# Optimization experiments

Hardware: AMD Instinct MI355X
Metric: run time of the kernel (lower is better)

The kernel has to match this reference:

```python
import jax, jax.numpy as jnp
import numpy as np
from jax import lax

B, CIN, COUT, H, W = 4, 256, 256, 64, 64
K = 3  # kernel size
PAD = 1
STRIDE = 1


def setup_inputs() -> dict:
    key = jax.random.key(0)
    k1, k2, k3, k4 = jax.random.split(key, 4)
    x = jax.random.normal(k1, (B, CIN, H, W), dtype=jnp.float32)
    # small offset weights so learned offsets are modest (original init is zeros)
    offset_w = jax.random.normal(k2, (3 * K * K, CIN, K, K), dtype=jnp.float32) * 0.01
    offset_b = jax.random.normal(k3, (3 * K * K,), dtype=jnp.float32) * 0.01
    dcn_w = jax.random.normal(k4, (COUT, CIN, K, K), dtype=jnp.float32) * (1.0 / np.sqrt(CIN * K * K))
    return {"x": x, "offset_w": offset_w, "offset_b": offset_b, "dcn_w": dcn_w}


def _dcnv2(x, offset_w, offset_b, dcn_w):
    b, c, h, w = x.shape
    kk = K * K
    # offset conv (standard 3x3, stride 1, pad 1)
    o = lax.conv_general_dilated(
        x, offset_w, (STRIDE, STRIDE), ((PAD, PAD), (PAD, PAD)),
        dimension_numbers=("NCHW", "OIHW", "NCHW"))
    o = o + offset_b[None, :, None, None]
    ho, wo = o.shape[2], o.shape[3]
    off = o[:, : 2 * kk].reshape(b, kk, 2, ho, wo)  # pairs are (dy, dx)
    dy, dx = off[:, :, 0], off[:, :, 1]             # [b,kk,ho,wo]
    mask = jax.nn.sigmoid(o[:, 2 * kk:])            # [b,kk,ho,wo]

    ki, kj = jnp.meshgrid(jnp.arange(K), jnp.arange(K), indexing="ij")
    ki = ki.reshape(kk).astype(jnp.float32)
    kj = kj.reshape(kk).astype(jnp.float32)
    base_y = (jnp.arange(ho, dtype=jnp.float32) * STRIDE - PAD)[None, None, :, None] + ki[None, :, None, None]
    base_x = (jnp.arange(wo, dtype=jnp.float32) * STRIDE - PAD)[None, None, None, :] + kj[None, :, None, None]
    py = base_y + dy  # [b,kk,ho,wo] sampling y
    px = base_x + dx  # sampling x

    y0 = jnp.floor(py)
    x0 = jnp.floor(px)
    wy = py - y0  # bilinear fractional weights
    wx = px - x0
    y0i = y0.astype(jnp.int32)
    x0i = x0.astype(jnp.int32)

    xT = x.transpose(0, 2, 3, 1)  # [b,h,w,c] for channel-last gathers
    bidx = jnp.arange(b)[:, None, None, None]

    def gather(yi, xi):
        # zero padding outside the image
        valid = (yi >= 0) & (yi < h) & (xi >= 0) & (xi < w)
        yc = jnp.clip(yi, 0, h - 1)
        xc = jnp.clip(xi, 0, w - 1)
        v = xT[bidx, yc, xc]  # [b,kk,ho,wo,c]
        return v * valid[..., None].astype(x.dtype)

    g00 = gather(y0i, x0i)
    g01 = gather(y0i, x0i + 1)
    g10 = gather(y0i + 1, x0i)
    g11 = gather(y0i + 1, x0i + 1)

    wy_ = wy[..., None]
    wx_ = wx[..., None]
    sampled = (g00 * (1 - wy_) * (1 - wx_) + g01 * (1 - wy_) * wx_
               + g10 * wy_ * (1 - wx_) + g11 * wy_ * wx_)
    sampled = sampled * mask[..., None]  # modulation

    wk = dcn_w.reshape(dcn_w.shape[0], c, kk)  # [o,c,kk]
    return jnp.einsum("bkhwc,ock->bohw", sampled, wk)


def reference(x, offset_w, offset_b, dcn_w):
    return _dcnv2(x, offset_w, offset_b, dcn_w)
```

## Files before the change

kernel.cpp:

```cpp
#include <hip/hip_runtime.h>
#include <hip/hip_bf16.h>
#include <stdint.h>
#include <math.h>

#define KDIM 2304

typedef __attribute__((ext_vector_type(8))) short bf16x8;
typedef __attribute__((ext_vector_type(4))) float f32x4;

__device__ inline unsigned short f2bf(float f) {
  union { float f; unsigned int u; } v; v.f = f;
  unsigned int u = v.u;
  unsigned int r = (u + 0x7FFFu + ((u >> 16) & 1u)) >> 16;
  return (unsigned short)r;
}
__device__ inline float bf2f(unsigned short h) {
  union { unsigned int u; float f; } v; v.u = ((unsigned int)h) << 16;
  return v.f;
}

__device__ inline void gl2lds16(const void* g, void* l) {
  __builtin_amdgcn_global_load_lds((const __attribute__((address_space(1))) void*)g,
                                   (__attribute__((address_space(3))) void*)l,
                                   16, 0, 0);
}

__global__ __launch_bounds__(256) void k_prep(const float* __restrict__ x,
                                              unsigned short* __restrict__ xTb,
                                              const float* __restrict__ dcn_w,
                                              const float* __restrict__ offset_w,
                                              unsigned short* __restrict__ Wpk,
                                              unsigned short* __restrict__ Wob,
                                              unsigned short* __restrict__ zp) {
  __shared__ float tile[32][33];
  int bx = (int)blockIdx.x;
  int t = threadIdx.x;
  if (bx < 4096) {
    int tx = t & 31, ty = t >> 5;
    int p0 = (bx & 127) * 32;
    int c0 = ((bx >> 7) & 7) * 32;
    int b  = bx >> 10;
    const float* xb = x + ((size_t)b << 20);
#pragma unroll
    for (int i = 0; i < 4; ++i) {
      int c = c0 + ty + i * 8;
      tile[ty + i * 8][tx] = xb[((size_t)c << 12) + p0 + tx];
    }
    __syncthreads();
    unsigned short* ob = xTb + ((size_t)b << 20);
#pragma unroll
    for (int i = 0; i < 4; ++i) {
      int p = p0 + ty + i * 8;
      ob[(((size_t)p) << 8) + c0 + tx] = f2bf(tile[tx][ty + i * 8]);
    }
  } else {
    int gid = (bx - 4096) * 256 + t;
    const int N1 = 72 * 8192;
    const int N2 = 32 * KDIM;
    if (gid < N1) {
      int j = gid & 7;
      int lane = (gid >> 3) & 63;
      int mb = (gid >> 9) & 15;
      int kc = gid >> 13;
      int row = mb * 16 + (lane & 15);
      int gk = kc * 32 + ((lane >> 4) << 3) + j;
      int c = gk & 255, kidx = gk >> 8;
      Wpk[gid] = f2bf(dcn_w[((size_t)(row * 256 + c)) * 9 + kidx]);
    } else if (gid < N1 + N2) {
      int g = gid - N1;
      int ch = g / KDIM, k = g % KDIM;
      int kidx = k >> 8, c = k & 255;
      Wob[g] = (ch < 27) ? f2bf(offset_w[((size_t)(ch * 256 + c)) * 9 + kidx])
                         : (unsigned short)0;
    } else if (gid < N1 + N2 + 128) {
      zp[gid - N1 - N2] = 0;
    }
  }
}

__global__ __launch_bounds__(512) void k_offs(const unsigned short* __restrict__ xTb,
                                              const unsigned short* __restrict__ Wob,
                                              const unsigned short* __restrict__ zp,
                                              const float* __restrict__ offb,
                                              float* __restrict__ SW) {
  __shared__ unsigned short As[2][64 * 32];
  __shared__ unsigned short Bs[2][32 * 32];
  __shared__ float Os[64][33];
  int t = threadIdx.x;
  int wv = t >> 6, lane = t & 63;
  int bid = (int)blockIdx.x;
  int swz = (bid & 7) * 32 + (bid >> 3);
  int n0 = swz * 64;
  int r0 = t >> 2, coff = (t & 3) * 8;

  int rowA = n0 + (r0 & 63);
  int b_ = rowA >> 12, hw = rowA & 4095, h = hw >> 6, w = hw & 63;

  f32x4 acc = {};

  auto stage = [&](int kt, int buf) {
    int k0 = kt * 32;
    int kidx = k0 >> 8, c0 = k0 & 255;
    if (t < 256) {
      int di = kidx / 3 - 1, dj = kidx % 3 - 1;
      int y = h + di, xx = w + dj;
      const unsigned short* g = (y >= 0 && y < 64 && xx >= 0 && xx < 64)
          ? xTb + (((((size_t)b_) << 12) + (y << 6) + xx) << 8) + c0 + coff
          : zp;
      gl2lds16(g, (char*)As[buf] + wv * 1024);
    } else if (t < 384) {
      int tt = t - 256;
      const unsigned short* gB = Wob + (size_t)(tt >> 2) * KDIM + k0 + (tt & 3) * 8;
      gl2lds16(gB, (char*)Bs[buf] + (wv - 4) * 1024);
    }
  };

  stage(0, 0);

  int mf = wv & 3, nf = wv >> 2;
  for (int kt = 0; kt < 72; ++kt) {
    int buf = kt & 1;
    if (kt + 1 < 72) {
      stage(kt + 1, buf ^ 1);
      if (t < 384) asm volatile("s_waitcnt vmcnt(1)" ::: "memory");
      else         asm volatile("s_waitcnt vmcnt(0)" ::: "memory");
    } else {
      asm volatile("s_waitcnt vmcnt(0)" ::: "memory");
    }
    asm volatile("s_barrier" ::: "memory");

    bf16x8 aF = *(const bf16x8*)(As[buf] + (mf * 16 + (lane & 15)) * 32 + (lane >> 4) * 8);
    bf16x8 bF = *(const bf16x8*)(Bs[buf] + (nf * 16 + (lane & 15)) * 32 + (lane >> 4) * 8);
    acc = __builtin_amdgcn_mfma_f32_16x16x32_bf16(aF, bF, acc, 0, 0, 0);

    asm volatile("s_barrier" ::: "memory");
  }

  int quad = lane >> 4, cl = lane & 15;
#pragma unroll
  for (int r = 0; r < 4; ++r)
    Os[mf * 16 + quad * 4 + r][nf * 16 + cl] = acc[r];
  __syncthreads();

  for (int item = t; item < 576; item += 512) {
    int bl = item & 63, k = item >> 6;
    int bhw = n0 + bl;
    int h_ = (bhw >> 6) & 63, w_ = bhw & 63;
    float dy = Os[bl][2 * k]     + offb[2 * k];
    float dx = Os[bl][2 * k + 1] + offb[2 * k + 1];
    float mv = Os[bl][18 + k]    + offb[18 + k];
    float mask = 1.0f / (1.0f + expf(-mv));

    float py = (float)(h_ - 1 + k / 3) + dy;
    float px = (float)(w_ - 1 + k % 3) + dx;
    float y0f = floorf(py), x0f = floorf(px);
    float wy = py - y0f, wx = px - x0f;
    int y0 = (int)y0f, x0 = (int)x0f;
    int y1 = y0 + 1, x1 = x0 + 1;

    float vy0 = (y0 >= 0 && y0 < 64) ? 1.f : 0.f;
    float vy1 = (y1 >= 0 && y1 < 64) ? 1.f : 0.f;
    float vx0 = (x0 >= 0 && x0 < 64) ? 1.f : 0.f;
    float vx1 = (x1 >= 0 && x1 < 64) ? 1.f : 0.f;
    int y0c = min(max(y0, 0), 63), y1c = min(max(y1, 0), 63);
    int x0c = min(max(x0, 0), 63), x1c = min(max(x1, 0), 63);

    float4 wv4;
    wv4.x = (1.f - wy) * (1.f - wx) * vy0 * vx0 * mask;
    wv4.y = (1.f - wy) * wx * vy0 * vx1 * mask;
    wv4.z = wy * (1.f - wx) * vy1 * vx0 * mask;
    wv4.w = wy * wx * vy1 * vx1 * mask;
    uint4 ov;
    ov.x = (unsigned)(((y0c << 6) + x0c) << 8);
    ov.y = (unsigned)(((y0c << 6) + x1c) << 8);
    ov.z = (unsigned)(((y1c << 6) + x0c) << 8);
    ov.w = (unsigned)(((y1c << 6) + x1c) << 8);

    float* p = SW + (size_t)(k * 16384 + bhw) * 8;
    *(float4*)p = wv4;
    *(uint4*)(p + 4) = ov;
  }
}

#define FSTEP(KT, Q, AF, BUF, DOSW)                                            \
  do {                                                                         \
    float s0_ = wv4.x * bf2f(Q[0].x) + wv4.y * bf2f(Q[1].x) +                  \
                wv4.z * bf2f(Q[2].x) + wv4.w * bf2f(Q[3].x);                   \
    float s1_ = wv4.x * bf2f(Q[0].y) + wv4.y * bf2f(Q[1].y) +                  \
                wv4.z * bf2f(Q[2].y) + wv4.w * bf2f(Q[3].y);                   \
    float s2_ = wv4.x * bf2f(Q[0].z) + wv4.y * bf2f(Q[1].z) +                  \
                wv4.z * bf2f(Q[2].z) + wv4.w * bf2f(Q[3].z);                   \
    float s3_ = wv4.x * bf2f(Q[0].w) + wv4.y * bf2f(Q[1].w) +                  \
                wv4.z * bf2f(Q[2].w) + wv4.w * bf2f(Q[3].w);                   \
    union { __hip_bfloat162 h2[2]; ushort4 v; } pk_;                           \
    pk_.h2[0] = __float22bfloat162_rn(make_float2(s0_, s1_));                  \
    pk_.h2[1] = __float22bfloat162_rn(make_float2(s2_, s3_));                  \
    *(ushort4*)(&Bs[BUF][bsw]) = pk_.v;                                        \
    if (DOSW && ((KT) & 7) == 0 && (KT) < 64) {                                \
      const float* swp_ =                                                      \
          SW + ((size_t)(((((KT) >> 3) + 1) << 14) + n0 + r)) * 8;             \
      wv4n = *(const float4*)swp_;                                             \
      ovn  = *(const uint4*)(swp_ + 4);                                        \
    }                                                                          \
    if ((KT) < 70) {                                                           \
      int kn_ = (KT) + 2;                                                      \
      uint4 o_ = (((KT) & 7) >= 6) ? ovn : ov;                                 \
      unsigned c_ = (unsigned)(((kn_ & 7) << 5) + ch0);                        \
      Q[0] = *(const ushort4*)(xb + o_.x + c_);                                \
      Q[1] = *(const ushort4*)(xb + o_.y + c_);                                \
      Q[2] = *(const ushort4*)(xb + o_.z + c_);                                \
      Q[3] = *(const ushort4*)(xb + o_.w + c_);                                \
    }                                                                          \
    asm volatile("s_waitcnt lgkmcnt(0)\n\ts_barrier" ::: "memory");            \
    bf16x8 bF0_ = *(const bf16x8*)(&Bs[BUF][(wn * 32 + (lane & 15)) * 40 +     \
                                            (lane >> 4) * 8]);                 \
    bf16x8 bF1_ = *(const bf16x8*)(&Bs[BUF][(wn * 32 + 16 + (lane & 15)) * 40 +\
                                            (lane >> 4) * 8]);                 \
    _Pragma("unroll")                                                          \
    for (int i_ = 0; i_ < 4; ++i_) {                                           \
      acc[i_][0] =                                                             \
          __builtin_amdgcn_mfma_f32_16x16x32_bf16(AF[i_], bF0_, acc[i_][0],    \
                                                  0, 0, 0);                    \
      acc[i_][1] =                                                             \
          __builtin_amdgcn_mfma_f32_16x16x32_bf16(AF[i_], bF1_, acc[i_][1],    \
                                                  0, 0, 0);                    \
    }                                                                          \
    if ((KT) < 70) {                                                           \
      int kn_ = (KT) + 2;                                                      \
      _Pragma("unroll")                                                        \
      for (int i_ = 0; i_ < 4; ++i_)                                           \
        AF[i_] = *(const bf16x8*)(wpBase + ((size_t)kn_ * 16 + i_) * 512);     \
    }                                                                          \
  } while (0)

__global__ __launch_bounds__(512) void k_fused(const unsigned short* __restrict__ Wpk,
                                               const unsigned short* __restrict__ xTb,
                                               const float* __restrict__ SW,
                                               float* __restrict__ out) {
  __shared__ __align__(16) unsigned short Bs[2][64 * 40];
  int t = threadIdx.x;
  int wv = t >> 6, lane = t & 63;
  int wm = wv & 3, wn = wv >> 2;
  int bid = (int)blockIdx.x;
  int swz = (bid & 7) * 32 + (bid >> 3);
  int n0 = swz * 64;
  int b  = n0 >> 12;
  const unsigned short* xb = xTb + ((size_t)b << 20);

  int r = t >> 3, g = t & 7;
  int ch0 = g * 4;
  int bsw = r * 40 + ch0;

  const unsigned short* wpBase = Wpk + ((size_t)(wm * 4 * 64 + lane)) * 8;

  f32x4 acc[4][2] = {};

  float4 wv4, wv4n; uint4 ov, ovn;
  {
    const float* sw = SW + ((size_t)(n0 + r)) * 8;
    wv4 = *(const float4*)sw;
    ov  = *(const uint4*)(sw + 4);
  }
  wv4n = wv4; ovn = ov;

  ushort4 qA[4], qB[4];
  bf16x8 aFA[4], aFB[4];

  {
    unsigned c0_ = (unsigned)ch0;
    qA[0] = *(const ushort4*)(xb + ov.x + c0_);
    qA[1] = *(const ushort4*)(xb + ov.y + c0_);
    qA[2] = *(const ushort4*)(xb + ov.z + c0_);
    qA[3] = *(const ushort4*)(xb + ov.w + c0_);
    unsigned c1_ = (unsigned)(32 + ch0);
    qB[0] = *(const ushort4*)(xb + ov.x + c1_);
    qB[1] = *(const ushort4*)(xb + ov.y + c1_);
    qB[2] = *(const ushort4*)(xb + ov.z + c1_);
    qB[3] = *(const ushort4*)(xb + ov.w + c1_);
#pragma unroll
    for (int i = 0; i < 4; ++i) {
      aFA[i] = *(const bf16x8*)(wpBase + (size_t)i * 512);
      aFB[i] = *(const bf16x8*)(wpBase + (size_t)(16 + i) * 512);
    }
  }

  for (int kt = 0; kt < 72; kt += 2) {
    FSTEP(kt,     qA, aFA, 0, 1);
    FSTEP(kt + 1, qB, aFB, 1, 0);
    if ((kt & 7) == 6) { wv4 = wv4n; ov = ovn; }
  }

  int quad = lane >> 4, cl = lane & 15;
  float* ob = out + (((size_t)b) << 20);
#pragma unroll
  for (int i = 0; i < 4; ++i) {
    int mbase = wm * 64 + i * 16 + quad * 4;
#pragma unroll
    for (int j = 0; j < 2; ++j) {
      int hw = (n0 & 4095) + wn * 32 + j * 16 + cl;
      float* op = ob + hw;
#pragma unroll
      for (int rr = 0; rr < 4; ++rr)
        op[((size_t)(mbase + rr)) << 12] = acc[i][j][rr];
    }
  }
}

extern "C" void kernel_launch(void* const* d_in, const int* in_sizes, int n_in,
                              void* d_out, int out_size, void* d_ws, size_t ws_size,
                              hipStream_t stream) {
  const float* x        = (const float*)d_in[0];
  const float* offset_w = (const float*)d_in[1];
  const float* offset_b = (const float*)d_in[2];
  const float* dcn_w    = (const float*)d_in[3];
  float* out = (float*)d_out;

  char* ws = (char*)d_ws;
  size_t off = 0;
  auto carve = [&](size_t bytes) -> void* {
    void* p = ws + off;
    off += (bytes + 255) & ~(size_t)255;
    return p;
  };
  unsigned short* xTb = (unsigned short*)carve(4ull * 64 * 64 * 256 * 2);
  unsigned short* Wpk = (unsigned short*)carve(72ull * 8192 * 2);
  unsigned short* Wob = (unsigned short*)carve(32ull * KDIM * 2);
  unsigned short* zp  = (unsigned short*)carve(256);
  float*          SW  = (float*)carve(9ull * 16384 * 8 * 4);
  (void)ws_size; (void)in_sizes; (void)n_in; (void)out_size;

  const int WPREP_BLOCKS = (72 * 8192 + 32 * KDIM + 128 + 255) / 256;
  k_prep<<<dim3(4096 + WPREP_BLOCKS), 256, 0, stream>>>(
      x, xTb, dcn_w, offset_w, Wpk, Wob, zp);
  k_offs<<<dim3(256), 512, 0, stream>>>(xTb, Wob, zp, offset_b, SW);
  k_fused<<<dim3(256), 512, 0, stream>>>(Wpk, xTb, SW, out);
}
```

Measured before the change: 147.8 us.

## Deepen offset-conv GEMM pipeline to 4 stages and vectorize transpose

The offset-conv GEMM kernel now uses 32-row tiles with 256 threads and 512 blocks. It prefetches three K-steps ahead into a 4-deep LDS ring, which removes the second barrier per iteration. The transpose prep kernel handles 64 channels per block with float4 loads and ushort4 bf16 stores, halving its block count. The aim is to hide global-load latency in the offset GEMM, spread it across more CUs, and cut memory-transaction count in the transpose. The cost is more outstanding loads per thread and more LDS per block.

Result: faster. 142.9 us (-3.3%).

```diff
diff --git a/kernel.cpp b/kernel.cpp
--- a/kernel.cpp
+++ b/kernel.cpp
@@ -32,29 +32,38 @@
                                               unsigned short* __restrict__ Wpk,
                                               unsigned short* __restrict__ Wob,
                                               unsigned short* __restrict__ zp) {
-  __shared__ float tile[32][33];
+  __shared__ float tile[32][65];
   int bx = (int)blockIdx.x;
   int t = threadIdx.x;
-  if (bx < 4096) {
-    int tx = t & 31, ty = t >> 5;
-    int p0 = (bx & 127) * 32;
-    int c0 = ((bx >> 7) & 7) * 32;
-    int b  = bx >> 10;
+  if (bx < 2048) {
+    int pt = bx & 127, ct = (bx >> 7) & 3, b = bx >> 9;
+    int p0 = pt * 32, c0 = ct * 64;
     const float* xb = x + ((size_t)b << 20);
 #pragma unroll
-    for (int i = 0; i < 4; ++i) {
-      int c = c0 + ty + i * 8;
-      tile[ty + i * 8][tx] = xb[((size_t)c << 12) + p0 + tx];
+    for (int i = 0; i < 2; ++i) {
+      int idx = t + i * 256;
+      int c = idx >> 3, pq = idx & 7;
+      float4 v = *(const float4*)(xb + ((size_t)(c0 + c) << 12) + p0 + pq * 4);
+      tile[pq * 4 + 0][c] = v.x;
+      tile[pq * 4 + 1][c] = v.y;
+      tile[pq * 4 + 2][c] = v.z;
+      tile[pq * 4 + 3][c] = v.w;
     }
     __syncthreads();
     unsigned short* ob = xTb + ((size_t)b << 20);
 #pragma unroll
-    for (int i = 0; i < 4; ++i) {
-      int p = p0 + ty + i * 8;
-      ob[(((size_t)p) << 8) + c0 + tx] = f2bf(tile[tx][ty + i * 8]);
+    for (int i = 0; i < 2; ++i) {
+      int idx = t + i * 256;
+      int p = idx >> 4, cg = idx & 15;
+      ushort4 o;
+      o.x = f2bf(tile[p][cg * 4 + 0]);
+      o.y = f2bf(tile[p][cg * 4 + 1]);
+      o.z = f2bf(tile[p][cg * 4 + 2]);
+      o.w = f2bf(tile[p][cg * 4 + 3]);
+      *(ushort4*)(ob + (((size_t)(p0 + p)) << 8) + c0 + cg * 4) = o;
     }
   } else {
-    int gid = (bx - 4096) * 256 + t;
+    int gid = (bx - 2048) * 256 + t;
     const int N1 = 72 * 8192;
     const int N2 = 32 * KDIM;
     if (gid < N1) {
@@ -78,62 +87,57 @@
   }
 }
 
-__global__ __launch_bounds__(512) void k_offs(const unsigned short* __restrict__ xTb,
+__global__ __launch_bounds__(256) void k_offs(const unsigned short* __restrict__ xTb,
                                               const unsigned short* __restrict__ Wob,
                                               const unsigned short* __restrict__ zp,
                                               const float* __restrict__ offb,
                                               float* __restrict__ SW) {
-  __shared__ unsigned short As[2][64 * 32];
-  __shared__ unsigned short Bs[2][32 * 32];
-  __shared__ float Os[64][33];
+  __shared__ unsigned short As[4][32 * 32];
+  __shared__ unsigned short Bs[4][32 * 32];
+  __shared__ float Os[32][33];
   int t = threadIdx.x;
   int wv = t >> 6, lane = t & 63;
   int bid = (int)blockIdx.x;
-  int swz = (bid & 7) * 32 + (bid >> 3);
-  int n0 = swz * 64;
-  int r0 = t >> 2, coff = (t & 3) * 8;
-
-  int rowA = n0 + (r0 & 63);
+  int swz = (bid & 7) * 64 + (bid >> 3);
+  int n0 = swz * 32;
+
+  int r0 = (t >> 2) & 31, coff = (t & 3) * 8;
+  int rowA = n0 + r0;
   int b_ = rowA >> 12, hw = rowA & 4095, h = hw >> 6, w = hw & 63;
+  int rB = ((t - 128) >> 2) & 31;
 
   f32x4 acc = {};
 
-  auto stage = [&](int kt, int buf) {
+  auto stage = [&](int kt) {
+    int buf = kt & 3;
     int k0 = kt * 32;
     int kidx = k0 >> 8, c0 = k0 & 255;
-    if (t < 256) {
+    if (t < 128) {
       int di = kidx / 3 - 1, dj = kidx % 3 - 1;
       int y = h + di, xx = w + dj;
       const unsigned short* g = (y >= 0 && y < 64 && xx >= 0 && xx < 64)
           ? xTb + (((((size_t)b_) << 12) + (y << 6) + xx) << 8) + c0 + coff
           : zp;
       gl2lds16(g, (char*)As[buf] + wv * 1024);
-    } else if (t < 384) {
-      int tt = t - 256;
-      const unsigned short* gB = Wob + (size_t)(tt >> 2) * KDIM + k0 + (tt & 3) * 8;
-      gl2lds16(gB, (char*)Bs[buf] + (wv - 4) * 1024);
+    } else {
+      const unsigned short* gB = Wob + (size_t)rB * KDIM + k0 + coff;
+      gl2lds16(gB, (char*)Bs[buf] + (wv - 2) * 1024);
     }
   };
 
-  stage(0, 0);
-
-  int mf = wv & 3, nf = wv >> 2;
+  stage(0); stage(1); stage(2);
+
+  int mf = wv & 1, nf = wv >> 1;
   for (int kt = 0; kt < 72; ++kt) {
-    int buf = kt & 1;
-    if (kt + 1 < 72) {
-      stage(kt + 1, buf ^ 1);
-      if (t < 384) asm volatile("s_waitcnt vmcnt(1)" ::: "memory");
-      else         asm volatile("s_waitcnt vmcnt(0)" ::: "memory");
-    } else {
-      asm volatile("s_waitcnt vmcnt(0)" ::: "memory");
-    }
+    if (kt <= 69)      asm volatile("s_waitcnt vmcnt(2)" ::: "memory");
+    else if (kt == 70) asm volatile("s_waitcnt vmcnt(1)" ::: "memory");
+    else               asm volatile("s_waitcnt vmcnt(0)" ::: "memory");
     asm volatile("s_barrier" ::: "memory");
-
+    if (kt + 3 < 72) stage(kt + 3);
+    int buf = kt & 3;
     bf16x8 aF = *(const bf16x8*)(As[buf] + (mf * 16 + (lane & 15)) * 32 + (lane >> 4) * 8);
     bf16x8 bF = *(const bf16x8*)(Bs[buf] + (nf * 16 + (lane & 15)) * 32 + (lane >> 4) * 8);
     acc = __builtin_amdgcn_mfma_f32_16x16x32_bf16(aF, bF, acc, 0, 0, 0);
-
-    asm volatile("s_barrier" ::: "memory");
   }
 
   int quad = lane >> 4, cl = lane & 15;
@@ -142,8 +146,8 @@
     Os[mf * 16 + quad * 4 + r][nf * 16 + cl] = acc[r];
   __syncthreads();
 
-  for (int item = t; item < 576; item += 512) {
-    int bl = item & 63, k = item >> 6;
+  for (int item = t; item < 288; item += 256) {
+    int bl = item & 31, k = item >> 5;
     int bhw = n0 + bl;
     int h_ = (bhw >> 6) & 63, w_ = bhw & 63;
     float dy = Os[bl][2 * k]     + offb[2 * k];
@@ -330,8 +334,8 @@
   (void)ws_size; (void)in_sizes; (void)n_in; (void)out_size;
 
   const int WPREP_BLOCKS = (72 * 8192 + 32 * KDIM + 128 + 255) / 256;
-  k_prep<<<dim3(4096 + WPREP_BLOCKS), 256, 0, stream>>>(
+  k_prep<<<dim3(2048 + WPREP_BLOCKS), 256, 0, stream>>>(
       x, xTb, dcn_w, offset_w, Wpk, Wob, zp);
-  k_offs<<<dim3(256), 512, 0, stream>>>(xTb, Wob, zp, offset_b, SW);
+  k_offs<<<dim3(512), 256, 0, stream>>>(xTb, Wob, zp, offset_b, SW);
   k_fused<<<dim3(256), 512, 0, stream>>>(Wpk, xTb, SW, out);
 }
```
